# Kernel optimization log

Hardware: AMD Instinct MI355X
Metric: run time of the kernel (lower is better)

## Reference

```python
import jax, jax.numpy as jnp
from jax import lax
import numpy as np

B, N, C = 4, 2048, 64          # batch, num points, feature channels
M = 512                         # num centroids (FPS)
SAMPLES = (32, 64)              # neighbors per scale
RADII = (0.2, 0.4)              # ball radii per scale
MLPS = ((67, 64, 64, 128), (67, 128, 128, 256))  # in->hidden->out per scale (in = C + 3)


def setup_inputs() -> dict:
    key = jax.random.key(0)
    ks = jax.random.split(key, 16)
    inp = {
        "points": jax.random.uniform(ks[0], (B, 3, N), jnp.float32),   # unit cube
        "features": jax.random.normal(ks[1], (B, C, N), jnp.float32),
    }
    k = 2
    for s, dims in enumerate(MLPS):
        for l in range(3):
            cin, cout = dims[l], dims[l + 1]
            inp[f"w{s}_{l}"] = (jax.random.normal(ks[k], (cout, cin), jnp.float32)
                                * jnp.float32(1.0 / np.sqrt(cin)))
            inp[f"b{s}_{l}"] = jnp.zeros((cout,), jnp.float32)
            k += 1
    return inp


def fps(xyz, m):
    """Farthest point sampling. xyz: (B,N,3) -> indices (B,m) int32."""
    b, n, _ = xyz.shape
    big = jnp.asarray(1e10, xyz.dtype)

    def step(carry, _):
        dist, cur = carry                                   # (B,N), (B,)
        cur_pt = jnp.take_along_axis(xyz, cur[:, None, None], axis=1)  # (B,1,3)
        d2 = jnp.sum((xyz - cur_pt) ** 2, axis=-1)          # (B,N)
        dist = jnp.minimum(dist, d2)
        nxt = jnp.argmax(dist, axis=-1).astype(jnp.int32)
        return (dist, nxt), cur

    init = (jnp.full((b, n), big, xyz.dtype), jnp.zeros((b,), jnp.int32))
    _, idxs = lax.scan(step, init, None, length=m)          # (m,B)
    return idxs.T                                           # (B,m)


def ball_group(xyz, feat_t, cent, s, r):
    """Ball query + group gather. Returns (B,M,s,3+C) = [rel_xyz; features]."""
    n = xyz.shape[1]
    d2 = jnp.sum((cent[:, :, None, :] - xyz[:, None, :, :]) ** 2, axis=-1)  # (B,M,N)
    keys = jnp.where(d2 <= r * r, jnp.arange(n, dtype=jnp.int32), n)
    idx = jnp.sort(keys, axis=-1)[:, :, :s]                 # first s in-ball indices
    idx = jnp.where(idx < n, idx, idx[:, :, :1])            # pad with first valid
    gxyz = jax.vmap(lambda p, i: p[i])(xyz, idx) - cent[:, :, None, :]  # (B,M,s,3)
    gfeat = jax.vmap(lambda f, i: f[i])(feat_t, idx)        # (B,M,s,C)
    return jnp.concatenate([gxyz, gfeat], axis=-1)


def mlp_max(g, ws, bs):
    """Shared 1x1-conv MLP over (B,M,S,Cin), max over neighbor dim S."""
    x = g
    for w, b in zip(ws, bs):
        x = jax.nn.relu(jnp.einsum('bmsc,oc->bmso', x, w) + b)
    return jnp.max(x, axis=2)                               # (B,M,Cout)


def reference(points, features,
              w0_0, b0_0, w0_1, b0_1, w0_2, b0_2,
              w1_0, b1_0, w1_1, b1_1, w1_2, b1_2):
    xyz = jnp.transpose(points, (0, 2, 1))                  # (B,N,3)
    feat_t = jnp.transpose(features, (0, 2, 1))             # (B,N,C)
    idx = fps(xyz, M)                                       # (B,M)
    cent = jnp.take_along_axis(xyz, idx[:, :, None], axis=1)  # (B,M,3)
    Ws = [(w0_0, w0_1, w0_2), (w1_0, w1_1, w1_2)]
    Bs = [(b0_0, b0_1, b0_2), (b1_0, b1_1, b1_2)]
    outs = []
    for i, (s, r) in enumerate(zip(SAMPLES, RADII)):
        g = ball_group(xyz, feat_t, cent, s, r)             # (B,M,s,3+C)
        outs.append(mlp_max(g, Ws[i], Bs[i]))               # (B,M,Cout_i)
    feat = jnp.transpose(jnp.concatenate(outs, axis=-1), (0, 2, 1))  # (B,384,M)
    return jnp.transpose(cent, (0, 2, 1)), feat             # (B,3,M), (B,384,M)
```

## Files before the change

kernel.cpp:

```cpp
#include <hip/hip_runtime.h>

#define NPTS 2048
#define BATCH 4
#define CFEAT 64
#define MCENT 512
#define NWORKERS 512
#define GRID_TOTAL (NWORKERS + 4)
#define NITEMS 4096
#define PROG_MAGIC 0xC5A70000u

typedef float f4 __attribute__((ext_vector_type(4)));
typedef float f2 __attribute__((ext_vector_type(2)));
typedef short s8v __attribute__((ext_vector_type(8)));

__device__ __forceinline__ unsigned short f2bf(float x) {
    unsigned u = __float_as_uint(x);
    return (unsigned short)((u + 0x7fffu + ((u >> 16) & 1u)) >> 16);
}

template <int CTRL>
__device__ __forceinline__ float dpp_max_step(float v) {
    int t = __builtin_amdgcn_update_dpp(0, __float_as_int(v), CTRL, 0xf, 0xf, true);
    return fmaxf(v, __int_as_float(t));
}

__device__ __forceinline__ float readlane_f(float v, int l) {
    return __int_as_float(__builtin_amdgcn_readlane(__float_as_int(v), l));
}

template <int COUT, int CIN, int KPW, bool PERM>
__device__ void pack_seg(const float* w, unsigned short* dst, int start, int stride) {
    for (int i = start; i < COUT * KPW; i += stride) {
        int o = i / KPW, k = i - o * KPW;
        float v = 0.f;
        if (PERM) {
            if (k < 64) v = w[o * CIN + 3 + k];
            else if (k < 67) v = w[o * CIN + (k - 64)];
        } else {
            if (k < CIN) v = w[o * CIN + k];
        }
        dst[i] = f2bf(v);
    }
}

__device__ void fps_body(int b, char* smem, const float* __restrict__ pts,
                         float* cent, unsigned int* prog, float* out)
{
    const int tid = threadIdx.x;
    const int lane = tid & 63, wv = tid >> 6;
    const float* px = pts + b * 3 * NPTS;
    const float* py = px + NPTS;
    const float* pz = py + NPTS;
    float4* scent = (float4*)smem;
    float4* slotq = (float4*)(smem + 8192);

    __builtin_amdgcn_s_setprio(3);

    const int base = wv * 512 + lane * 8;
    f2 rx[4], ry[4], rz[4], rd[4];
#pragma unroll
    for (int i = 0; i < 4; ++i) {
        rx[i] = *(const f2*)(px + base + 2 * i);
        ry[i] = *(const f2*)(py + base + 2 * i);
        rz[i] = *(const f2*)(pz + base + 2 * i);
        rd[i] = (f2){1e10f, 1e10f};
    }
    float cx = px[0], cy = py[0], cz = pz[0];
    int par = 0;
    for (int m = 0; m < MCENT; ++m) {
        if (tid == 0) scent[m] = make_float4(cx, cy, cz, 0.f);
        if (wv == 0 && lane < 48 && (m & 15) == 15) {
            int mm = m - 15 + lane / 3;
            int comp = lane - (lane / 3) * 3;
            float val = ((float*)&scent[mm])[comp];
            cent[(b * MCENT + mm) * 3 + comp] = val;
        }
        if (tid == 0 && (m & 15) == 1 && m > 16)
            __hip_atomic_store(&prog[b], PROG_MAGIC | (unsigned)(m - 1),
                               __ATOMIC_RELEASE, __HIP_MEMORY_SCOPE_AGENT);
        {
#pragma clang fp contract(off)
            f2 c2x = {cx, cx}, c2y = {cy, cy}, c2z = {cz, cz};
#pragma unroll
            for (int i = 0; i < 4; ++i) {
                f2 dx = rx[i] - c2x, dy = ry[i] - c2y, dz = rz[i] - c2z;
                f2 d2 = dx * dx + dy * dy;
                d2 = d2 + dz * dz;
                f2 old = rd[i];
                f2 nd;
                nd.x = fminf(old.x, d2.x);
                nd.y = fminf(old.y, d2.y);
                rd[i] = nd;
            }
        }
        float n0 = rd[0].x, n1 = rd[0].y, n2 = rd[1].x, n3 = rd[1].y;
        float n4 = rd[2].x, n5 = rd[2].y, n6 = rd[3].x, n7 = rd[3].y;
        float bv = fmaxf(fmaxf(fmaxf(n0, n1), fmaxf(n2, n3)),
                         fmaxf(fmaxf(n4, n5), fmaxf(n6, n7)));
        float ox = rx[3].y, oy = ry[3].y, oz = rz[3].y;
        {
            float ndv[8] = {n0, n1, n2, n3, n4, n5, n6, n7};
#pragma unroll
            for (int k = 6; k >= 0; --k) {
                bool t = (ndv[k] == bv);
                float nx = (k & 1) ? rx[k >> 1].y : rx[k >> 1].x;
                float ny = (k & 1) ? ry[k >> 1].y : ry[k >> 1].x;
                float nz = (k & 1) ? rz[k >> 1].y : rz[k >> 1].x;
                ox = t ? nx : ox; oy = t ? ny : oy; oz = t ? nz : oz;
            }
        }
        float v = bv;
        v = dpp_max_step<0x111>(v);
        v = dpp_max_step<0x112>(v);
        v = dpp_max_step<0x114>(v);
        v = dpp_max_step<0x118>(v);
        v = dpp_max_step<0x142>(v);
        v = dpp_max_step<0x143>(v);
        float wmax = readlane_f(v, 63);
        unsigned long long cand = __ballot(bv == wmax);
        int wl = __ffsll(cand) - 1;
        if (lane == wl) slotq[(par * 4 + wv) * 2] = make_float4(bv, ox, oy, oz);
        __syncthreads();
        float4 s0 = slotq[(par * 4 + 0) * 2];
        float4 s1 = slotq[(par * 4 + 1) * 2];
        float4 s2 = slotq[(par * 4 + 2) * 2];
        float4 s3 = slotq[(par * 4 + 3) * 2];
        float4 c01 = (s1.x > s0.x) ? s1 : s0;
        float4 c23 = (s3.x > s2.x) ? s3 : s2;
        float4 cc  = (c23.x > c01.x) ? c23 : c01;
        cx = cc.y; cy = cc.z; cz = cc.w;
        par ^= 1;
    }
    if (tid == 0)
        __hip_atomic_store(&prog[b], PROG_MAGIC | 512u,
                           __ATOMIC_RELEASE, __HIP_MEMORY_SCOPE_AGENT);
    __syncthreads();
    float* outc = out + b * 3 * MCENT;
    for (int mm = tid; mm < MCENT; mm += 256) {
        float4 c = scent[mm];
        outc[mm] = c.x; outc[MCENT + mm] = c.y; outc[2 * MCENT + mm] = c.z;
    }
}

template <int MT, int KSTEPS, int NTW>
__device__ __forceinline__ void layer_mm(const unsigned short* A, const unsigned short* __restrict__ Wg,
                                         const float* __restrict__ bias, int lane, int wv,
                                         f4 (&acc)[MT][NTW])
{
    constexpr int KP = KSTEPS * 32;
    const int r15 = lane & 15, g = lane >> 4;
#pragma unroll
    for (int nt = 0; nt < NTW; ++nt) {
        int n = (wv * NTW + nt) * 16 + r15;
        float bv = bias[n];
#pragma unroll
        for (int mt = 0; mt < MT; ++mt) acc[mt][nt] = (f4){bv, bv, bv, bv};
    }
#pragma unroll
    for (int ks = 0; ks < KSTEPS; ++ks) {
        s8v afr[MT];
#pragma unroll
        for (int mt = 0; mt < MT; ++mt) {
            int row = mt * 16 + r15;
            int byte = ((row * KP + ks * 32 + g * 8) * 2) ^ ((row & 7) << 4);
            afr[mt] = *(const s8v*)((const char*)A + byte);
        }
#pragma unroll
        for (int nt = 0; nt < NTW; ++nt) {
            int n = (wv * NTW + nt) * 16 + r15;
            s8v bfr = *(const s8v*)(Wg + n * KP + ks * 32 + g * 8);
#pragma unroll
            for (int mt = 0; mt < MT; ++mt)
                acc[mt][nt] = __builtin_amdgcn_mfma_f32_16x16x32_bf16(afr[mt], bfr, acc[mt][nt], 0, 0, 0);
        }
    }
}

template <int MT, int NTW, int CO>
__device__ __forceinline__ void store_lds(f4 (&acc)[MT][NTW], unsigned short* OUT, int lane, int wv) {
    const int r15 = lane & 15, g = lane >> 4;
#pragma unroll
    for (int mt = 0; mt < MT; ++mt)
#pragma unroll
        for (int nt = 0; nt < NTW; ++nt)
#pragma unroll
            for (int q = 0; q < 4; ++q) {
                int j = mt * 16 + g * 4 + q;
                int n = (wv * NTW + nt) * 16 + r15;
                float v = fmaxf(acc[mt][nt][q], 0.f);
                int byte = ((j * CO + n) * 2) ^ ((j & 7) << 4);
                *(unsigned short*)((char*)OUT + byte) = f2bf(v);
            }
}

template <int S_, int C1, int C2, int C3>
__device__ __forceinline__ void msg_body(int bm, char* smem,
    const float* __restrict__ pts, const unsigned short* __restrict__ ftr,
    const float* __restrict__ cent,
    const unsigned short* __restrict__ W0, const float* __restrict__ B0,
    const unsigned short* __restrict__ W1, const float* __restrict__ B1,
    const unsigned short* __restrict__ W2, const float* __restrict__ B2,
    float* __restrict__ outf, int ch_off, float rr)
{
    constexpr int MT = S_ / 16;
    constexpr int KS1 = C1 / 32, KS2 = C2 / 32;
    constexpr int NW1 = C1 / 64, NW2 = C2 / 64, NW3 = C3 / 64;
    constexpr int HA = (S_ * 96 > S_ * C2) ? S_ * 96 : S_ * C2;
    unsigned short* hA = (unsigned short*)smem;
    unsigned short* hB = hA + HA;
    int* nbr = (int*)(hB + S_ * C1);
    int* wtot = nbr + S_;
    const int tid = threadIdx.x, lane = tid & 63, wv = tid >> 6;
    const int b = bm >> 9, m = bm & (MCENT - 1);
    const float cx = cent[bm * 3], cy = cent[bm * 3 + 1], cz = cent[bm * 3 + 2];
    const float* px = pts + b * 3 * NPTS;
    const float* py = px + NPTS;
    const float* pz = py + NPTS;

    unsigned mask = 0; int cnt = 0;
    {
#pragma clang fp contract(off)
#pragma unroll
        for (int k = 0; k < 8; ++k) {
            int n = tid * 8 + k;
            float dx = cx - px[n], dy = cy - py[n], dz = cz - pz[n];
            float d2 = dx * dx + dy * dy;
            d2 = d2 + dz * dz;
            if (d2 <= rr) { mask |= 1u << k; ++cnt; }
        }
    }
    int inc = cnt;
#pragma unroll
    for (int off = 1; off < 64; off <<= 1) {
        int t = __shfl_up(inc, off);
        if (lane >= off) inc += t;
    }
    if (lane == 63) wtot[wv] = inc;
    __syncthreads();
    int base = 0, tot = 0;
#pragma unroll
    for (int w = 0; w < 4; ++w) { int t = wtot[w]; tot += t; if (w < wv) base += t; }
    int pos = base + inc - cnt;
#pragma unroll
    for (int k = 0; k < 8; ++k) {
        if ((mask >> k) & 1) {
            if (pos < S_) nbr[pos] = tid * 8 + k;
            ++pos;
        }
    }
    __syncthreads();
    const int first = nbr[0];

    for (int e = tid; e < S_ * 8; e += 256) {
        int j = e >> 3, c8 = e & 7;
        int p = (j < tot) ? nbr[j] : first;
        s8v v = *(const s8v*)(ftr + (b * NPTS + p) * 64 + c8 * 8);
        int byte = ((j * 96 + c8 * 8) * 2) ^ ((j & 7) << 4);
        *(s8v*)((char*)hA + byte) = v;
    }
    for (int e = tid; e < S_ * 4; e += 256) {
        int j = e >> 2, q = e & 3;
        int p = (j < tot) ? nbr[j] : first;
        s8v v = {0, 0, 0, 0, 0, 0, 0, 0};
        if (q == 0) {
            v[0] = (short)f2bf(px[p] - cx);
            v[1] = (short)f2bf(py[p] - cy);
            v[2] = (short)f2bf(pz[p] - cz);
        }
        int byte = ((j * 96 + 64 + q * 8) * 2) ^ ((j & 7) << 4);
        *(s8v*)((char*)hA + byte) = v;
    }
    __syncthreads();

    {
        f4 acc[MT][NW1];
        layer_mm<MT, 3, NW1>(hA, W0, B0, lane, wv, acc);
        store_lds<MT, NW1, C1>(acc, hB, lane, wv);
    }
    __syncthreads();
    {
        f4 acc[MT][NW2];
        layer_mm<MT, KS1, NW2>(hB, W1, B1, lane, wv, acc);
        store_lds<MT, NW2, C2>(acc, hA, lane, wv);
    }
    __syncthreads();
    {
        f4 acc[MT][NW3];
        layer_mm<MT, KS2, NW3>(hA, W2, B2, lane, wv, acc);
        const int r15 = lane & 15;
        float* dst = outf + b * 384 * MCENT + ch_off * MCENT + m;
#pragma unroll
        for (int nt = 0; nt < NW3; ++nt) {
            float mv = -1e30f;
#pragma unroll
            for (int mt = 0; mt < MT; ++mt)
#pragma unroll
                for (int q = 0; q < 4; ++q) mv = fmaxf(mv, acc[mt][nt][q]);
            mv = fmaxf(mv, __shfl_xor(mv, 16));
            mv = fmaxf(mv, __shfl_xor(mv, 32));
            float v = fmaxf(mv, 0.f);
            if (lane < 16) dst[((wv * NW3 + nt) * 16 + r15) * MCENT] = v;
        }
    }
}

__global__ __launch_bounds__(256, 4) void fused(
    const float* __restrict__ pts, const float* __restrict__ feats,
    const float* w00, const float* b00, const float* w01, const float* b01,
    const float* w02, const float* b02, const float* w10, const float* b10,
    const float* w11, const float* b11, const float* w12, const float* b12,
    float* cent, unsigned short* ftr, unsigned short* wp,
    unsigned long long* pmask, unsigned int* prog,
    float* out, float* outf, float rr0, float rr1)
{
    extern __shared__ __align__(16) char smem[];
    const int blk = blockIdx.x;
    const int tid = threadIdx.x;

    if (blk < 4) {
        fps_body(blk, smem, pts, cent, prog, out);
        return;
    }
    const int w = blk - 4;
    if (w < 64) {
        const int stride = 64 * 256;
        const int start = w * 256 + tid;
        for (int i = start; i < BATCH * NPTS * CFEAT; i += stride) {
            int c = i & 63, n = (i >> 6) & (NPTS - 1), b = i >> 17;
            ftr[i] = f2bf(feats[(b * CFEAT + c) * NPTS + n]);
        }
        pack_seg<64, 67, 96, true>(w00, wp + 0, start, stride);
        pack_seg<64, 64, 64, false>(w01, wp + 6144, start, stride);
        pack_seg<128, 64, 64, false>(w02, wp + 10240, start, stride);
        pack_seg<128, 67, 96, true>(w10, wp + 18432, start, stride);
        pack_seg<128, 128, 128, false>(w11, wp + 30720, start, stride);
        pack_seg<256, 128, 128, false>(w12, wp + 47104, start, stride);
        __syncthreads();
        if (tid == 0)
            __hip_atomic_fetch_or(pmask, 1ull << w, __ATOMIC_RELEASE, __HIP_MEMORY_SCOPE_AGENT);
    }

    bool prep_ok = false;
    for (int i = w; i < NITEMS; i += NWORKERS) {
        int m = i >> 3, sub = i & 7;
        int b = sub & 3, scale = sub >> 2;
        if (tid == 0) {
            if (!prep_ok) {
                while (__hip_atomic_load(pmask, __ATOMIC_ACQUIRE, __HIP_MEMORY_SCOPE_AGENT) != ~0ull)
                    __builtin_amdgcn_s_sleep(32);
            }
            for (;;) {
                unsigned p = __hip_atomic_load(&prog[b], __ATOMIC_ACQUIRE, __HIP_MEMORY_SCOPE_AGENT);
                if ((p & 0xFFFF0000u) == PROG_MAGIC && (p & 0xFFFFu) > (unsigned)m) break;
                __builtin_amdgcn_s_sleep(127);
            }
        }
        prep_ok = true;
        __syncthreads();
        int bm = (b << 9) | m;
        if (scale == 0)
            msg_body<32, 64, 64, 128>(bm, smem, pts, ftr, cent,
                                      wp + 0, b00, wp + 6144, b01, wp + 10240, b02, outf, 0, rr0);
        else
            msg_body<64, 128, 128, 256>(bm, smem, pts, ftr, cent,
                                        wp + 18432, b10, wp + 30720, b11, wp + 47104, b12, outf, 128, rr1);
    }
}

extern "C" void kernel_launch(void* const* d_in, const int* in_sizes, int n_in,
                              void* d_out, int out_size, void* d_ws, size_t ws_size,
                              hipStream_t stream) {
    const float* pts  = (const float*)d_in[0];
    const float* feats = (const float*)d_in[1];
    const float* w00 = (const float*)d_in[2];  const float* b00 = (const float*)d_in[3];
    const float* w01 = (const float*)d_in[4];  const float* b01 = (const float*)d_in[5];
    const float* w02 = (const float*)d_in[6];  const float* b02 = (const float*)d_in[7];
    const float* w10 = (const float*)d_in[8];  const float* b10 = (const float*)d_in[9];
    const float* w11 = (const float*)d_in[10]; const float* b11 = (const float*)d_in[11];
    const float* w12 = (const float*)d_in[12]; const float* b12 = (const float*)d_in[13];
    float* out = (float*)d_out;
    char* ws = (char*)d_ws;
    float* cent = (float*)ws;
    unsigned short* ftr = (unsigned short*)(ws + 24576);
    unsigned short* wp  = (unsigned short*)(ws + 24576 + 1048576);
    unsigned long long* pmask = (unsigned long long*)(ws + 24576 + 1048576 + 159744);
    unsigned int* prog = (unsigned int*)(ws + 24576 + 1048576 + 159744 + 8);

    float* outf = out + BATCH * 3 * MCENT;
    const float RR0 = (float)(0.2 * 0.2);
    const float RR1 = (float)(0.4 * 0.4);
    hipLaunchKernelGGL(fused, dim3(GRID_TOTAL), dim3(256), 33040, stream,
                       pts, feats, w00, b00, w01, b01, w02, b02, w10, b10, w11, b11, w12, b12,
                       cent, ftr, wp, pmask, prog, out, outf, RR0, RR1);
}
```

Before: 329.6 us.

## Defer workers sharing a CU with FPS blocks and use cache-bypassing sync loads

Each FPS block writes its hardware CU/XCC id to a signal array. Worker blocks read these ids, and any worker co-resident on the same CU as an FPS block waits until FPS has fully finished before doing work, so it does not steal cycles from the latency-critical serial FPS loop. Progress and centroid traffic switches from agent-scope atomics to inline-asm sc0 sc1 loads and stores with explicit waitcnt. This relies on hardware-register ids and hand-written memory ordering. Stale signal values from a previous launch could match, and deferred workers may end up idle.

```diff
diff --git a/kernel.cpp b/kernel.cpp
--- a/kernel.cpp
+++ b/kernel.cpp
@@ -8,6 +8,7 @@
 #define GRID_TOTAL (NWORKERS + 4)
 #define NITEMS 4096
 #define PROG_MAGIC 0xC5A70000u
+#define SIG_MAGIC  0xA5B00000u
 
 typedef float f4 __attribute__((ext_vector_type(4)));
 typedef float f2 __attribute__((ext_vector_type(2)));
@@ -26,6 +27,25 @@
 
 __device__ __forceinline__ float readlane_f(float v, int l) {
     return __int_as_float(__builtin_amdgcn_readlane(__float_as_int(v), l));
+}
+
+__device__ __forceinline__ unsigned load_sc01(const unsigned* p) {
+    unsigned v;
+    asm volatile("global_load_dword %0, %1, off sc0 sc1\n\ts_waitcnt vmcnt(0)"
+                 : "=v"(v) : "v"(p) : "memory");
+    return v;
+}
+__device__ __forceinline__ float loadf_sc01(const float* p) {
+    float v;
+    asm volatile("global_load_dword %0, %1, off sc0 sc1\n\ts_waitcnt vmcnt(0)"
+                 : "=v"(v) : "v"(p) : "memory");
+    return v;
+}
+__device__ __forceinline__ void store_sc01(unsigned* p, unsigned v) {
+    asm volatile("global_store_dword %0, %1, off sc0 sc1" :: "v"(p), "v"(v) : "memory");
+}
+__device__ __forceinline__ void storef_sc01(float* p, float v) {
+    asm volatile("global_store_dword %0, %1, off sc0 sc1" :: "v"(p), "v"(v) : "memory");
 }
 
 template <int COUT, int CIN, int KPW, bool PERM>
@@ -73,11 +93,12 @@
             int mm = m - 15 + lane / 3;
             int comp = lane - (lane / 3) * 3;
             float val = ((float*)&scent[mm])[comp];
-            cent[(b * MCENT + mm) * 3 + comp] = val;
-        }
-        if (tid == 0 && (m & 15) == 1 && m > 16)
-            __hip_atomic_store(&prog[b], PROG_MAGIC | (unsigned)(m - 1),
-                               __ATOMIC_RELEASE, __HIP_MEMORY_SCOPE_AGENT);
+            storef_sc01(cent + (b * MCENT + mm) * 3 + comp, val);
+        }
+        if (tid == 0 && (m & 15) == 1 && m > 16) {
+            asm volatile("s_waitcnt vmcnt(0)" ::: "memory");
+            store_sc01(&prog[b], PROG_MAGIC | (unsigned)(m - 1));
+        }
         {
 #pragma clang fp contract(off)
             f2 c2x = {cx, cx}, c2y = {cy, cy}, c2z = {cz, cz};
@@ -131,9 +152,10 @@
         cx = cc.y; cy = cc.z; cz = cc.w;
         par ^= 1;
     }
-    if (tid == 0)
-        __hip_atomic_store(&prog[b], PROG_MAGIC | 512u,
-                           __ATOMIC_RELEASE, __HIP_MEMORY_SCOPE_AGENT);
+    if (tid == 0) {
+        asm volatile("s_waitcnt vmcnt(0)" ::: "memory");
+        store_sc01(&prog[b], PROG_MAGIC | 512u);
+    }
     __syncthreads();
     float* outc = out + b * 3 * MCENT;
     for (int mm = tid; mm < MCENT; mm += 256) {
@@ -212,7 +234,9 @@
     int* wtot = nbr + S_;
     const int tid = threadIdx.x, lane = tid & 63, wv = tid >> 6;
     const int b = bm >> 9, m = bm & (MCENT - 1);
-    const float cx = cent[bm * 3], cy = cent[bm * 3 + 1], cz = cent[bm * 3 + 2];
+    const float cx = loadf_sc01(cent + bm * 3);
+    const float cy = loadf_sc01(cent + bm * 3 + 1);
+    const float cz = loadf_sc01(cent + bm * 3 + 2);
     const float* px = pts + b * 3 * NPTS;
     const float* py = px + NPTS;
     const float* pz = py + NPTS;
@@ -310,14 +334,20 @@
     const float* w02, const float* b02, const float* w10, const float* b10,
     const float* w11, const float* b11, const float* w12, const float* b12,
     float* cent, unsigned short* ftr, unsigned short* wp,
-    unsigned long long* pmask, unsigned int* prog,
+    unsigned long long* pmask, unsigned int* prog, unsigned int* sig,
     float* out, float* outf, float rr0, float rr1)
 {
     extern __shared__ __align__(16) char smem[];
+    __shared__ unsigned sdefer;
     const int blk = blockIdx.x;
     const int tid = threadIdx.x;
 
     if (blk < 4) {
+        if (tid == 0) {
+            unsigned hwid = __builtin_amdgcn_s_getreg(63492);
+            unsigned xcc  = __builtin_amdgcn_s_getreg(63508);
+            store_sc01(&sig[blk], SIG_MAGIC | ((xcc & 7u) << 8) | ((hwid >> 8) & 0xFFu));
+        }
         fps_body(blk, smem, pts, cent, prog, out);
         return;
     }
@@ -340,6 +370,25 @@
             __hip_atomic_fetch_or(pmask, 1ull << w, __ATOMIC_RELEASE, __HIP_MEMORY_SCOPE_AGENT);
     }
 
+    if (tid == 0) {
+        unsigned hwid = __builtin_amdgcn_s_getreg(63492);
+        unsigned xcc  = __builtin_amdgcn_s_getreg(63508);
+        unsigned myid = SIG_MAGIC | ((xcc & 7u) << 8) | ((hwid >> 8) & 0xFFu);
+        unsigned d = 0;
+        for (int s = 0; s < 4; ++s) {
+            unsigned sv;
+            for (;;) {
+                sv = load_sc01(&sig[s]);
+                if ((sv & 0xFFF00000u) == SIG_MAGIC) break;
+                __builtin_amdgcn_s_sleep(16);
+            }
+            d |= (sv == myid) ? 1u : 0u;
+        }
+        sdefer = d;
+    }
+    __syncthreads();
+    const bool defer = sdefer != 0;
+
     bool prep_ok = false;
     for (int i = w; i < NITEMS; i += NWORKERS) {
         int m = i >> 3, sub = i & 7;
@@ -349,9 +398,10 @@
                 while (__hip_atomic_load(pmask, __ATOMIC_ACQUIRE, __HIP_MEMORY_SCOPE_AGENT) != ~0ull)
                     __builtin_amdgcn_s_sleep(32);
             }
+            unsigned need = defer ? 512u : (unsigned)(m + 1);
             for (;;) {
-                unsigned p = __hip_atomic_load(&prog[b], __ATOMIC_ACQUIRE, __HIP_MEMORY_SCOPE_AGENT);
-                if ((p & 0xFFFF0000u) == PROG_MAGIC && (p & 0xFFFFu) > (unsigned)m) break;
+                unsigned p = load_sc01(&prog[b]);
+                if ((p & 0xFFFF0000u) == PROG_MAGIC && (p & 0xFFFFu) >= need) break;
                 __builtin_amdgcn_s_sleep(127);
             }
         }
@@ -383,13 +433,15 @@
     float* cent = (float*)ws;
     unsigned short* ftr = (unsigned short*)(ws + 24576);
     unsigned short* wp  = (unsigned short*)(ws + 24576 + 1048576);
-    unsigned long long* pmask = (unsigned long long*)(ws + 24576 + 1048576 + 159744);
-    unsigned int* prog = (unsigned int*)(ws + 24576 + 1048576 + 159744 + 8);
+    char* sync_base = ws + 24576 + 1048576 + 159744;
+    unsigned long long* pmask = (unsigned long long*)sync_base;
+    unsigned int* prog = (unsigned int*)(sync_base + 8);
+    unsigned int* sig  = (unsigned int*)(sync_base + 24);
 
     float* outf = out + BATCH * 3 * MCENT;
     const float RR0 = (float)(0.2 * 0.2);
     const float RR1 = (float)(0.4 * 0.4);
     hipLaunchKernelGGL(fused, dim3(GRID_TOTAL), dim3(256), 33040, stream,
                        pts, feats, w00, b00, w01, b01, w02, b02, w10, b10, w11, b11, w12, b12,
-                       cent, ftr, wp, pmask, prog, out, outf, RR0, RR1);
-}
+                       cent, ftr, wp, pmask, prog, sig, out, outf, RR0, RR1);
+}
```

New measurement: 438.3 us. +33.0%, slower.
